# Performance work log

Hardware: AMD Instinct MI355X
Metric: run time of the kernel (lower is better)

Reference implementation:

```python
import jax, jax.numpy as jnp
import numpy as np

MUL0, MUL1 = 128, 64            # scalar (0e) and vector (1o) multiplicities
B = 8192                        # batch of nodes
SQRT3 = 3.0 ** 0.5
SQRT6 = 6.0 ** 0.5

# path normalization (e3nn 'component' irrep norm / 'element' path norm):
# coeff_ins = sqrt(dim(ir_out) / fan_in(i_out)), fan_in = sum_{ins -> i_out} mul1*mul2
A_0E = (1.0 / (MUL0 * MUL0 + MUL1 * MUL1)) ** 0.5   # paths (0,0,0)+(1,1,0)
A_1O = (3.0 / (MUL0 * MUL1 + MUL1 * MUL0)) ** 0.5   # paths (0,1,1)+(1,0,1)
A_1E = (3.0 / (MUL1 * MUL1)) ** 0.5                  # path  (1,1,1)


def _levi_civita():
    eps = np.zeros((3, 3, 3), dtype=np.float32)
    eps[0, 1, 2] = eps[1, 2, 0] = eps[2, 0, 1] = 1.0
    eps[0, 2, 1] = eps[2, 1, 0] = eps[1, 0, 2] = -1.0
    return jnp.asarray(eps)


def setup_inputs() -> dict:
    key = jax.random.key(0)
    ks = jax.random.split(key, 7)
    return {
        "x1": jax.random.normal(ks[0], (B, MUL0 + 3 * MUL1), dtype=jnp.float32),
        "x2": jax.random.normal(ks[1], (B, MUL0 + 3 * MUL1), dtype=jnp.float32),
        "w000": jax.random.normal(ks[2], (MUL0, MUL0, MUL0), dtype=jnp.float32),
        "w011": jax.random.normal(ks[3], (MUL0, MUL1, MUL1), dtype=jnp.float32),
        "w101": jax.random.normal(ks[4], (MUL1, MUL0, MUL1), dtype=jnp.float32),
        "w110": jax.random.normal(ks[5], (MUL1, MUL1, MUL0), dtype=jnp.float32),
        "w111": jax.random.normal(ks[6], (MUL1, MUL1, MUL1), dtype=jnp.float32),
    }


def reference(x1, x2, w000, w011, w101, w110, w111):
    b = x1.shape[0]
    # split irreps: scalars [b, 128], vectors [b, 64, 3]
    s1, v1 = x1[:, :MUL0], x1[:, MUL0:].reshape(b, MUL1, 3)
    s2, v2 = x2[:, :MUL0], x2[:, MUL0:].reshape(b, MUL1, 3)

    # 0e output: 0e x 0e -> 0e (w3j = 1) and 1o x 1o -> 0e (w3j = delta/sqrt3)
    out0 = A_0E * (
        jnp.einsum("uvw,bu,bv->bw", w000, s1, s2)
        + jnp.einsum("uvw,bui,bvi->bw", w110, v1, v2) / SQRT3
    )

    # 1o output: 0e x 1o -> 1o and 1o x 0e -> 1o (w3j = delta/sqrt3)
    out1o = (A_1O / SQRT3) * (
        jnp.einsum("uvw,bu,bvi->bwi", w011, s1, v2)
        + jnp.einsum("uvw,bui,bv->bwi", w101, v1, s2)
    )

    # 1e output: 1o x 1o -> 1e (w3j = levi-civita / sqrt6)
    eps = _levi_civita()
    out1e = (A_1E / SQRT6) * jnp.einsum("uvw,bui,bvj,ijk->bwk", w111, v1, v2, eps)

    return jnp.concatenate(
        [out0, out1o.reshape(b, -1), out1e.reshape(b, -1)], axis=-1
    )  # [b, 128 + 192 + 192] = [b, 512]
```

## Files before the change

### kernel.cpp

```cpp
#include <hip/hip_runtime.h>
#include <stdint.h>


typedef _Float16 f16;
typedef f16 f16x8 __attribute__((ext_vector_type(8)));
typedef float f32x4 __attribute__((ext_vector_type(4)));
typedef int i32x4 __attribute__((ext_vector_type(4)));

#define OFF_W000 0u
#define OFF_W110 2097152u
#define OFF_W011 2621440u
#define OFF_W101 3145728u
#define OFF_W111 3670016u
#define OFF_XS1  3932160u
#define OFF_XS2  4980736u
#define OFF_XV1  6029312u
#define OFF_XV2  7602176u
#define OFF_S0A  9175040u
#define OFF_S0B  10223616u
#define OFF_S1O  13369344u
#define WS_ELEMS 14942208u

#define SC_0E 0.006987712429686843f
#define SC_1O 0.0078125f
#define SC_1E 0.011048543456039806f

__global__ void tile_all_k(const float* __restrict__ w000, const float* __restrict__ w011,
                           const float* __restrict__ w101, const float* __restrict__ w110,
                           const float* __restrict__ w111, const float* __restrict__ x1,
                           const float* __restrict__ x2, f16* __restrict__ ws)
{
  unsigned tid = blockIdx.x*256u + threadIdx.x;
  if (tid < 2097152u) {
    unsigned e=tid&7u, n=(tid>>3)&63u, q=(tid>>9)&3u, p=(tid>>11)&1u,
             u=(tid>>12)&127u, vh=(tid>>19)&1u, h=(tid>>20)&1u;
    unsigned v = vh*64u + p*32u + q*8u + e;
    ws[OFF_W000+tid] = (f16)w000[u*16384u + v*128u + h*64u + n];
    return;
  }
  tid -= 2097152u;
  if (tid < 524288u) {
    unsigned e=tid&7u, n=(tid>>3)&63u, q=(tid>>9)&3u, p=(tid>>11)&1u,
             u=(tid>>12)&63u, h=(tid>>18)&1u;
    unsigned v = p*32u + q*8u + e;
    ws[OFF_W110+tid] = (f16)(w110[u*8192u + v*128u + h*64u + n] * 0.5773502691896258f);
    return;
  }
  tid -= 524288u;
  if (tid < 524288u) {
    unsigned e=tid&7u, n=(tid>>3)&63u, q=(tid>>9)&3u, p=(tid>>11)&1u, u=tid>>12;
    unsigned v = p*32u + q*8u + e;
    ws[OFF_W011+tid] = (f16)w011[u*4096u + v*64u + n];
    return;
  }
  tid -= 524288u;
  if (tid < 524288u) {
    unsigned e=tid&7u, n=(tid>>3)&63u, q=(tid>>9)&3u, p=(tid>>11)&1u, u=tid>>12;
    unsigned v = p*32u + q*8u + e;
    ws[OFF_W101+tid] = (f16)w101[v*8192u + u*64u + n];
    return;
  }
  tid -= 524288u;
  if (tid < 262144u) {
    unsigned e=tid&7u, n=(tid>>3)&63u, q=(tid>>9)&3u, p=(tid>>11)&1u, u=tid>>12;
    unsigned v = p*32u + q*8u + e;
    ws[OFF_W111+tid] = (f16)w111[u*4096u + v*64u + n];
    return;
  }
  tid -= 262144u;
  if (tid < 1048576u) {
    unsigned e=tid&7u, r=(tid>>3)&127u, uo=(tid>>10)&15u, rt=tid>>14;
    ws[OFF_XS1+tid] = (f16)x1[(rt*128u+r)*320u + uo*8u + e];
    return;
  }
  tid -= 1048576u;
  if (tid < 1572864u) {
    unsigned e=tid&7u, r=(tid>>3)&127u, ov=(tid>>10)&7u, rest=tid>>13;
    unsigned i=rest%3u, rt=rest/3u;
    ws[OFF_XV1+tid] = (f16)x1[(rt*128u+r)*320u + 128u + (ov*8u+e)*3u + i];
    return;
  }
  tid -= 1572864u;
  if (tid < 1048576u) {
    unsigned e=tid&7u, r=(tid>>3)&127u, uo=(tid>>10)&15u, rt=tid>>14;
    ws[OFF_XS2+tid] = (f16)x2[(rt*128u+r)*320u + uo*8u + e];
    return;
  }
  tid -= 1048576u;
  {
    unsigned e=tid&7u, r=(tid>>3)&127u, ov=(tid>>10)&7u, rest=tid>>13;
    unsigned i=rest%3u, rt=rest/3u;
    ws[OFF_XV2+tid] = (f16)x2[(rt*128u+r)*320u + 128u + (ov*8u+e)*3u + i];
  }
}

#define GLD16(g,l) __builtin_amdgcn_global_load_lds( \
    (const __attribute__((address_space(1))) unsigned int*)(g), \
    (__attribute__((address_space(3))) unsigned int*)(l), 16, 0, 0)

#define WAITV(n) asm volatile("s_waitcnt vmcnt(" #n ")" ::: "memory")

template<bool NEG, int SS>
__device__ __forceinline__ void run_phase(const f16* __restrict__ Wt,
    const f16* __restrict__ aW, const f16* __restrict__ bW, int bRow,
    f16* sWw, f16* sAw, f32x4 (&acc)[4][4], int lane)
{
  constexpr int M = SS*8;
  const int q = lane >> 4, r15 = lane & 15;

  f16x8 br[4][2];
#pragma unroll
  for (int mt=0; mt<4; ++mt)
#pragma unroll
    for (int o=0; o<2; ++o)
      br[mt][o] = *(const f16x8*)(bW + (o*4+q)*1024 + (bRow + mt*16 + r15)*8);
#pragma unroll
  for (int mt=0; mt<4; ++mt)
#pragma unroll
    for (int o=0; o<2; ++o) {
      i32x4 tmp = __builtin_bit_cast(i32x4, br[mt][o]);
      asm volatile("" :: "v"(tmp));
    }

  auto stPair = [&](int p, int slot){
    const char* s = (const char*)Wt + (size_t)p*8192;
    char* d = (char*)sWw + slot*8192;
#pragma unroll
    for (int c=0; c<8; ++c)
      GLD16(s + c*1024 + lane*16, d + c*1024);
  };
  auto stA = [&](int ss2){
    GLD16((const char*)(aW + ss2*1024) + lane*16, (char*)sAw + (ss2&1)*1024);
  };

  stPair(0,0); stA(0); stPair(1,1);

  f16x8 aR[4];
#pragma unroll 1
  for (int ss = 0; ss < SS; ++ss) {
#pragma unroll
    for (int kc = 0; kc < 8; ++kc) {
      const int t = ss*8 + kc;
      if (kc == 7) { if (ss+1 < SS) { WAITV(9); } else { WAITV(0); } }
      else         { WAITV(8); }
      if (kc == 0) {
#pragma unroll
        for (int mt=0; mt<4; ++mt)
          aR[mt] = *(const f16x8*)(sAw + (ss&1)*512 + (mt*16+r15)*8);
      }
      __builtin_amdgcn_s_setprio(1);
#pragma unroll
      for (int p=0; p<2; ++p) {
        f16x8 af[4];
#pragma unroll
        for (int mt=0; mt<4; ++mt) {
          f16 av = aR[mt][kc];
          if constexpr (NEG) av = -av;
          af[mt] = av * br[mt][p];
        }
#pragma unroll
        for (int nt=0; nt<4; ++nt) {
          f16x8 bw = *(const f16x8*)(sWw + (kc&1)*4096 + p*2048 + (q*64 + nt*16 + r15)*8);
#pragma unroll
          for (int mt=0; mt<4; ++mt)
            acc[mt][nt] = __builtin_amdgcn_mfma_f32_16x16x32_f16(af[mt], bw, acc[mt][nt], 0,0,0);
        }
      }
      __builtin_amdgcn_s_setprio(0);
      __builtin_amdgcn_sched_barrier(0);
      if (kc == 6 && ss+1 < SS) stA(ss+1);
      if (t + 2 < M) stPair(t+2, kc&1);
    }
  }
}

__global__ __launch_bounds__(256, 2)
void tp_main(f16* __restrict__ ws, float* __restrict__ out)
{
  __shared__ f16 smem[36864];
  const int lane = threadIdx.x & 63, wid = threadIdx.x >> 6;
  f16* sWw = smem + wid*8192;
  f16* sAw = smem + 32768 + wid*1024;
  const int q = lane >> 4, r15 = lane & 15;
  const int sub = wid >> 1, rh = wid & 1;

  f32x4 acc[4][4];
#pragma unroll
  for (int a=0;a<4;++a)
#pragma unroll
    for (int b=0;b<4;++b) acc[a][b] = (f32x4){0.f,0.f,0.f,0.f};

  const int bid = blockIdx.x;

#define STORE_DIRECT(base_col_expr, SC)                                   \
  _Pragma("unroll")                                                       \
  for (int mt=0;mt<4;++mt)                                                \
    _Pragma("unroll")                                                     \
    for (int nt=0;nt<4;++nt)                                              \
      _Pragma("unroll")                                                   \
      for (int rg=0;rg<4;++rg)                                            \
        out[(rowb+mt*16+q*4+rg)*512 + (base_col_expr)] = (SC)*acc[mt][nt][rg];

#define STORE_SLAB(slab, stride, col_expr, SC)                            \
  _Pragma("unroll")                                                       \
  for (int mt=0;mt<4;++mt)                                                \
    _Pragma("unroll")                                                     \
    for (int nt=0;nt<4;++nt)                                              \
      _Pragma("unroll")                                                   \
      for (int rg=0;rg<4;++rg)                                            \
        (slab)[(rowb+mt*16+q*4+rg)*(stride) + (col_expr)] = (f16)((SC)*acc[mt][nt][rg]);

  if (bid < 128) {
    const int rtp = bid >> 2, vh = (bid >> 1) & 1, h = bid & 1;
    const int rtt = rtp*2 + sub;
    const f16* aW = ws + OFF_XS1 + rtt*16384 + rh*512;
    const f16* bW = ws + OFF_XS2 + rtt*16384 + vh*8192;
    const f16* Wt = ws + OFF_W000 + h*1048576u + vh*524288u;
    run_phase<false,16>(Wt, aW, bW, rh*64, sWw, sAw, acc, lane);
    const int rowb = rtt*128 + rh*64;
    if (vh == 0) { STORE_DIRECT(h*64+nt*16+r15, SC_0E) }
    else { f16* slab = ws + OFF_S0A; STORE_SLAB(slab, 128, h*64+nt*16+r15, SC_0E) }
  } else if (bid < 224) {
    const int id = bid-128, i = id%3, rtp = id/3;
    const int rtt = rtp*2 + sub;
    const f16* aW = ws + OFF_XS1 + rtt*16384 + rh*512;
    const f16* bW = ws + OFF_XV2 + (rtt*3+i)*8192;
    run_phase<false,16>(ws + OFF_W011, aW, bW, rh*64, sWw, sAw, acc, lane);
    const int rowb = rtt*128 + rh*64;
    STORE_DIRECT(128 + 3*(nt*16+r15) + i, SC_1O)
  } else if (bid < 320) {
    const int id = bid-224, i = id%3, rtp = id/3;
    const int rtt = rtp*2 + sub;
    const f16* aW = ws + OFF_XS2 + rtt*16384 + rh*512;
    const f16* bW = ws + OFF_XV1 + (rtt*3+i)*8192;
    run_phase<false,16>(ws + OFF_W101, aW, bW, rh*64, sWw, sAw, acc, lane);
    const int rowb = rtt*128 + rh*64;
    f16* slab = ws + OFF_S1O;
    STORE_SLAB(slab, 192, 3*(nt*16+r15) + i, SC_1O)
  } else if (bid < 416) {
    const int id = bid-320, kk = id%3, rtp = id/3;
    int i = kk+1; if (i>2) i-=3;
    int j = kk+2; if (j>2) j-=3;
    const int rtt = rtp*2 + sub;
    run_phase<false,8>(ws + OFF_W111,
        ws + OFF_XV1 + (rtt*3+i)*8192 + rh*512, ws + OFF_XV2 + (rtt*3+j)*8192,
        rh*64, sWw, sAw, acc, lane);
    run_phase<true,8>(ws + OFF_W111,
        ws + OFF_XV1 + (rtt*3+j)*8192 + rh*512, ws + OFF_XV2 + (rtt*3+i)*8192,
        rh*64, sWw, sAw, acc, lane);
    const int rowb = rtt*128 + rh*64;
    STORE_DIRECT(320 + 3*(nt*16+r15) + kk, SC_1E)
  } else {
    const int id = bid-416, i = id%3, h = (id/3)&1, rtp = id/6;
    const int rtt = rtp*2 + sub;
    const f16* aW = ws + OFF_XV1 + (rtt*3+i)*8192 + rh*512;
    const f16* bW = ws + OFF_XV2 + (rtt*3+i)*8192;
    run_phase<false,8>(ws + OFF_W110 + h*262144u, aW, bW, rh*64, sWw, sAw, acc, lane);
    const int rowb = rtt*128 + rh*64;
    f16* slab = ws + OFF_S0B + (unsigned)i*1048576u;
    STORE_SLAB(slab, 128, h*64+nt*16+r15, SC_0E)
  }
#undef STORE_DIRECT
#undef STORE_SLAB
}

__global__ void ep_add(const f16* __restrict__ ws, float* __restrict__ out)
{
  unsigned tid = blockIdx.x*256u + threadIdx.x;
  if (tid < 1048576u) {
    unsigned r = tid>>7, c = tid&127u;
    float s = (float)ws[OFF_S0A+tid] + (float)ws[OFF_S0B+tid]
            + (float)ws[OFF_S0B+1048576u+tid] + (float)ws[OFF_S0B+2097152u+tid];
    out[r*512u+c] += s;
  } else {
    unsigned t2 = tid - 1048576u;
    unsigned r = t2/192u, c = t2 - r*192u;
    out[r*512u+128u+c] += (float)ws[OFF_S1O+t2];
  }
}

extern "C" void kernel_launch(void* const* d_in, const int* in_sizes, int n_in,
                              void* d_out, int out_size, void* d_ws, size_t ws_size,
                              hipStream_t stream)
{
  const float* x1   = (const float*)d_in[0];
  const float* x2   = (const float*)d_in[1];
  const float* w000 = (const float*)d_in[2];
  const float* w011 = (const float*)d_in[3];
  const float* w101 = (const float*)d_in[4];
  const float* w110 = (const float*)d_in[5];
  const float* w111 = (const float*)d_in[6];
  float* out = (float*)d_out;
  f16* ws   = (f16*)d_ws;

  if (ws_size < (size_t)WS_ELEMS * 2) return;

  tile_all_k<<<35840, 256, 0, stream>>>(w000, w011, w101, w110, w111, x1, x2, ws);
  tp_main<<<608, 256, 0, stream>>>(ws, out);
  ep_add<<<10240, 256, 0, stream>>>(ws, out);
}
```

Measured before the change: 157.6 us.

## Stream weights directly into registers with single-wave blocks, drop LDS staging

Replaces the LDS-staged weight pipeline (global_load_lds with double buffering across 4 waves) with per-wave direct global loads into a 4-deep register ring. The main kernel now launches many 64-thread blocks. Inputs are relaid out with rows contiguous across all nodes, and the w000 path is no longer split over the v halves, which removes the S0A partial slab. The epilogue reduction is rewritten for the new slab layout. The aim is to remove LDS traffic and barrier waits and to improve load balance, at the cost of more global and L2 traffic per wave and higher register pressure.

```diff
diff --git a/kernel.cpp b/kernel.cpp
--- a/kernel.cpp
+++ b/kernel.cpp
@@ -5,7 +5,6 @@
 typedef _Float16 f16;
 typedef f16 f16x8 __attribute__((ext_vector_type(8)));
 typedef float f32x4 __attribute__((ext_vector_type(4)));
-typedef int i32x4 __attribute__((ext_vector_type(4)));
 
 #define OFF_W000 0u
 #define OFF_W110 2097152u
@@ -16,10 +15,9 @@
 #define OFF_XS2  4980736u
 #define OFF_XV1  6029312u
 #define OFF_XV2  7602176u
-#define OFF_S0A  9175040u
-#define OFF_S0B  10223616u
-#define OFF_S1O  13369344u
-#define WS_ELEMS 14942208u
+#define OFF_S110 9175040u
+#define OFF_S101 12320768u
+#define WS_ELEMS 13893632u
 
 #define SC_0E 0.006987712429686843f
 #define SC_1O 0.0078125f
@@ -32,16 +30,16 @@
 {
   unsigned tid = blockIdx.x*256u + threadIdx.x;
   if (tid < 2097152u) {
-    unsigned e=tid&7u, n=(tid>>3)&63u, q=(tid>>9)&3u, p=(tid>>11)&1u,
-             u=(tid>>12)&127u, vh=(tid>>19)&1u, h=(tid>>20)&1u;
-    unsigned v = vh*64u + p*32u + q*8u + e;
+    unsigned e=tid&7u, n=(tid>>3)&63u, q=(tid>>9)&3u, vq=(tid>>11)&3u,
+             u=(tid>>13)&127u, h=tid>>20;
+    unsigned v = vq*32u + q*8u + e;
     ws[OFF_W000+tid] = (f16)w000[u*16384u + v*128u + h*64u + n];
     return;
   }
   tid -= 2097152u;
   if (tid < 524288u) {
     unsigned e=tid&7u, n=(tid>>3)&63u, q=(tid>>9)&3u, p=(tid>>11)&1u,
-             u=(tid>>12)&63u, h=(tid>>18)&1u;
+             u=(tid>>12)&63u, h=tid>>18;
     unsigned v = p*32u + q*8u + e;
     ws[OFF_W110+tid] = (f16)(w110[u*8192u + v*128u + h*64u + n] * 0.5773502691896258f);
     return;
@@ -69,196 +67,182 @@
   }
   tid -= 262144u;
   if (tid < 1048576u) {
-    unsigned e=tid&7u, r=(tid>>3)&127u, uo=(tid>>10)&15u, rt=tid>>14;
-    ws[OFF_XS1+tid] = (f16)x1[(rt*128u+r)*320u + uo*8u + e];
+    unsigned e=tid&7u, r=(tid>>3)&8191u, o=tid>>16;
+    ws[OFF_XS1+tid] = (f16)x1[r*320u + o*8u + e];
+    return;
+  }
+  tid -= 1048576u;
+  if (tid < 1048576u) {
+    unsigned e=tid&7u, r=(tid>>3)&8191u, o=tid>>16;
+    ws[OFF_XS2+tid] = (f16)x2[r*320u + o*8u + e];
     return;
   }
   tid -= 1048576u;
   if (tid < 1572864u) {
-    unsigned e=tid&7u, r=(tid>>3)&127u, ov=(tid>>10)&7u, rest=tid>>13;
-    unsigned i=rest%3u, rt=rest/3u;
-    ws[OFF_XV1+tid] = (f16)x1[(rt*128u+r)*320u + 128u + (ov*8u+e)*3u + i];
+    unsigned e=tid&7u, r=(tid>>3)&8191u, o=(tid>>16)&7u, i=tid>>19;
+    ws[OFF_XV1+tid] = (f16)x1[r*320u + 128u + (o*8u+e)*3u + i];
     return;
   }
   tid -= 1572864u;
-  if (tid < 1048576u) {
-    unsigned e=tid&7u, r=(tid>>3)&127u, uo=(tid>>10)&15u, rt=tid>>14;
-    ws[OFF_XS2+tid] = (f16)x2[(rt*128u+r)*320u + uo*8u + e];
-    return;
-  }
-  tid -= 1048576u;
   {
-    unsigned e=tid&7u, r=(tid>>3)&127u, ov=(tid>>10)&7u, rest=tid>>13;
-    unsigned i=rest%3u, rt=rest/3u;
-    ws[OFF_XV2+tid] = (f16)x2[(rt*128u+r)*320u + 128u + (ov*8u+e)*3u + i];
-  }
-}
-
-#define GLD16(g,l) __builtin_amdgcn_global_load_lds( \
-    (const __attribute__((address_space(1))) unsigned int*)(g), \
-    (__attribute__((address_space(3))) unsigned int*)(l), 16, 0, 0)
-
-#define WAITV(n) asm volatile("s_waitcnt vmcnt(" #n ")" ::: "memory")
-
-template<bool NEG, int SS>
-__device__ __forceinline__ void run_phase(const f16* __restrict__ Wt,
-    const f16* __restrict__ aW, const f16* __restrict__ bW, int bRow,
-    f16* sWw, f16* sAw, f32x4 (&acc)[4][4], int lane)
-{
-  constexpr int M = SS*8;
+    unsigned e=tid&7u, r=(tid>>3)&8191u, o=(tid>>16)&7u, i=tid>>19;
+    ws[OFF_XV2+tid] = (f16)x2[r*320u + 128u + (o*8u+e)*3u + i];
+  }
+}
+
+template<int VQ2, int SS, bool NEG>
+__device__ __forceinline__ void run_stream(
+    const f16* __restrict__ W, const f16* __restrict__ aP,
+    const f16* __restrict__ bP, int rowb, int lane, f32x4 (&acc)[4][4])
+{
+  constexpr int L = 8*VQ2;
   const int q = lane >> 4, r15 = lane & 15;
-
-  f16x8 br[4][2];
+  const int rbase = rowb + r15;
+
+  f16x8 br[4][VQ2];
 #pragma unroll
   for (int mt=0; mt<4; ++mt)
 #pragma unroll
-    for (int o=0; o<2; ++o)
-      br[mt][o] = *(const f16x8*)(bW + (o*4+q)*1024 + (bRow + mt*16 + r15)*8);
+    for (int vq=0; vq<VQ2; ++vq)
+      br[mt][vq] = *(const f16x8*)(bP + (unsigned)((vq*4+q)*8192 + rbase + mt*16)*8u);
+
+  const f16* Wl = W + (q*64 + r15)*8;
+  f16x8 ring[4][4];
+#pragma unroll
+  for (int s=0; s<4; ++s)
+#pragma unroll
+    for (int nt=0; nt<4; ++nt)
+      ring[s][nt] = *(const f16x8*)(Wl + s*2048 + nt*128);
+
+  f16x8 aR[4], aRn[4];
 #pragma unroll
   for (int mt=0; mt<4; ++mt)
-#pragma unroll
-    for (int o=0; o<2; ++o) {
-      i32x4 tmp = __builtin_bit_cast(i32x4, br[mt][o]);
-      asm volatile("" :: "v"(tmp));
+    aR[mt] = *(const f16x8*)(aP + (unsigned)(rbase + mt*16)*8u);
+
+#pragma unroll 1
+  for (int ss = 0; ss < SS-1; ++ss) {
+    const f16* Wss = Wl + (unsigned)(ss*L)*2048u;
+    const f16* An  = aP + (unsigned)((ss+1)*8192)*8u;
+#pragma unroll
+    for (int kc = 0; kc < L; ++kc) {
+      if (kc == L-6) {
+#pragma unroll
+        for (int mt=0; mt<4; ++mt)
+          aRn[mt] = *(const f16x8*)(An + (unsigned)(rbase + mt*16)*8u);
+      }
+      f16x8 af[4];
+#pragma unroll
+      for (int mt=0; mt<4; ++mt) {
+        f16 av = aR[mt][kc/VQ2];
+        if constexpr (NEG) av = -av;
+        af[mt] = av * br[mt][kc%VQ2];
+      }
+#pragma unroll
+      for (int nt=0; nt<4; ++nt)
+#pragma unroll
+        for (int mt=0; mt<4; ++mt)
+          acc[mt][nt] = __builtin_amdgcn_mfma_f32_16x16x32_f16(af[mt], ring[kc&3][nt], acc[mt][nt], 0,0,0);
+#pragma unroll
+      for (int nt=0; nt<4; ++nt)
+        ring[kc&3][nt] = *(const f16x8*)(Wss + (kc+4)*2048 + nt*128);
     }
-
-  auto stPair = [&](int p, int slot){
-    const char* s = (const char*)Wt + (size_t)p*8192;
-    char* d = (char*)sWw + slot*8192;
-#pragma unroll
-    for (int c=0; c<8; ++c)
-      GLD16(s + c*1024 + lane*16, d + c*1024);
-  };
-  auto stA = [&](int ss2){
-    GLD16((const char*)(aW + ss2*1024) + lane*16, (char*)sAw + (ss2&1)*1024);
-  };
-
-  stPair(0,0); stA(0); stPair(1,1);
-
-  f16x8 aR[4];
-#pragma unroll 1
-  for (int ss = 0; ss < SS; ++ss) {
-#pragma unroll
-    for (int kc = 0; kc < 8; ++kc) {
-      const int t = ss*8 + kc;
-      if (kc == 7) { if (ss+1 < SS) { WAITV(9); } else { WAITV(0); } }
-      else         { WAITV(8); }
-      if (kc == 0) {
+#pragma unroll
+    for (int mt=0; mt<4; ++mt) aR[mt] = aRn[mt];
+  }
+  {
+    const f16* Wss = Wl + (unsigned)((SS-1)*L)*2048u;
+#pragma unroll
+    for (int kc = 0; kc < L; ++kc) {
+      f16x8 af[4];
+#pragma unroll
+      for (int mt=0; mt<4; ++mt) {
+        f16 av = aR[mt][kc/VQ2];
+        if constexpr (NEG) av = -av;
+        af[mt] = av * br[mt][kc%VQ2];
+      }
+#pragma unroll
+      for (int nt=0; nt<4; ++nt)
 #pragma unroll
         for (int mt=0; mt<4; ++mt)
-          aR[mt] = *(const f16x8*)(sAw + (ss&1)*512 + (mt*16+r15)*8);
-      }
-      __builtin_amdgcn_s_setprio(1);
-#pragma unroll
-      for (int p=0; p<2; ++p) {
-        f16x8 af[4];
-#pragma unroll
-        for (int mt=0; mt<4; ++mt) {
-          f16 av = aR[mt][kc];
-          if constexpr (NEG) av = -av;
-          af[mt] = av * br[mt][p];
-        }
-#pragma unroll
-        for (int nt=0; nt<4; ++nt) {
-          f16x8 bw = *(const f16x8*)(sWw + (kc&1)*4096 + p*2048 + (q*64 + nt*16 + r15)*8);
-#pragma unroll
-          for (int mt=0; mt<4; ++mt)
-            acc[mt][nt] = __builtin_amdgcn_mfma_f32_16x16x32_f16(af[mt], bw, acc[mt][nt], 0,0,0);
-        }
-      }
-      __builtin_amdgcn_s_setprio(0);
-      __builtin_amdgcn_sched_barrier(0);
-      if (kc == 6 && ss+1 < SS) stA(ss+1);
-      if (t + 2 < M) stPair(t+2, kc&1);
+          acc[mt][nt] = __builtin_amdgcn_mfma_f32_16x16x32_f16(af[mt], ring[kc&3][nt], acc[mt][nt], 0,0,0);
+      if (kc < L-4) {
+#pragma unroll
+        for (int nt=0; nt<4; ++nt)
+          ring[kc&3][nt] = *(const f16x8*)(Wss + (kc+4)*2048 + nt*128);
+      }
     }
   }
 }
 
-__global__ __launch_bounds__(256, 2)
+__global__ __launch_bounds__(64, 2)
 void tp_main(f16* __restrict__ ws, float* __restrict__ out)
 {
-  __shared__ f16 smem[36864];
-  const int lane = threadIdx.x & 63, wid = threadIdx.x >> 6;
-  f16* sWw = smem + wid*8192;
-  f16* sAw = smem + 32768 + wid*1024;
+  const int lane = threadIdx.x & 63;
   const int q = lane >> 4, r15 = lane & 15;
-  const int sub = wid >> 1, rh = wid & 1;
 
   f32x4 acc[4][4];
 #pragma unroll
-  for (int a=0;a<4;++a)
-#pragma unroll
-    for (int b=0;b<4;++b) acc[a][b] = (f32x4){0.f,0.f,0.f,0.f};
-
-  const int bid = blockIdx.x;
-
-#define STORE_DIRECT(base_col_expr, SC)                                   \
+  for (int a=0; a<4; ++a)
+#pragma unroll
+    for (int b=0; b<4; ++b) acc[a][b] = (f32x4){0.f,0.f,0.f,0.f};
+
+  const int x = blockIdx.x & 7, r = blockIdx.x >> 3;
+
+#define STORE_DIRECT(col_expr, SC)                                        \
   _Pragma("unroll")                                                       \
   for (int mt=0;mt<4;++mt)                                                \
     _Pragma("unroll")                                                     \
     for (int nt=0;nt<4;++nt)                                              \
       _Pragma("unroll")                                                   \
       for (int rg=0;rg<4;++rg)                                            \
-        out[(rowb+mt*16+q*4+rg)*512 + (base_col_expr)] = (SC)*acc[mt][nt][rg];
-
-#define STORE_SLAB(slab, stride, col_expr, SC)                            \
+        out[(unsigned)(rowb+mt*16+q*4+rg)*512u + (unsigned)(col_expr)] = (SC)*acc[mt][nt][rg];
+
+#define STORE_SLAB(base, SC)                                              \
   _Pragma("unroll")                                                       \
   for (int mt=0;mt<4;++mt)                                                \
     _Pragma("unroll")                                                     \
     for (int nt=0;nt<4;++nt)                                              \
       _Pragma("unroll")                                                   \
       for (int rg=0;rg<4;++rg)                                            \
-        (slab)[(rowb+mt*16+q*4+rg)*(stride) + (col_expr)] = (f16)((SC)*acc[mt][nt][rg]);
-
-  if (bid < 128) {
-    const int rtp = bid >> 2, vh = (bid >> 1) & 1, h = bid & 1;
-    const int rtt = rtp*2 + sub;
-    const f16* aW = ws + OFF_XS1 + rtt*16384 + rh*512;
-    const f16* bW = ws + OFF_XS2 + rtt*16384 + vh*8192;
-    const f16* Wt = ws + OFF_W000 + h*1048576u + vh*524288u;
-    run_phase<false,16>(Wt, aW, bW, rh*64, sWw, sAw, acc, lane);
-    const int rowb = rtt*128 + rh*64;
-    if (vh == 0) { STORE_DIRECT(h*64+nt*16+r15, SC_0E) }
-    else { f16* slab = ws + OFF_S0A; STORE_SLAB(slab, 128, h*64+nt*16+r15, SC_0E) }
-  } else if (bid < 224) {
-    const int id = bid-128, i = id%3, rtp = id/3;
-    const int rtt = rtp*2 + sub;
-    const f16* aW = ws + OFF_XS1 + rtt*16384 + rh*512;
-    const f16* bW = ws + OFF_XV2 + (rtt*3+i)*8192;
-    run_phase<false,16>(ws + OFF_W011, aW, bW, rh*64, sWw, sAw, acc, lane);
-    const int rowb = rtt*128 + rh*64;
+        ws[(base) + (unsigned)(rowb+mt*16+q*4+rg)*64u + (unsigned)(nt*16+r15)] \
+            = (f16)((SC)*acc[mt][nt][rg]);
+
+  if (r < 32) {
+    const int j = x*32 + r, h = j >> 7, rg = j & 127;
+    const int rowb = rg*64;
+    run_stream<4,16,false>(ws + OFF_W000 + (unsigned)h*1048576u,
+                           ws + OFF_XS1, ws + OFF_XS2, rowb, lane, acc);
+    STORE_DIRECT(h*64 + nt*16 + r15, SC_0E)
+  } else if (r < 80) {
+    const int j = x*48 + (r-32), i = j/128, rg = j%128;
+    const int rowb = rg*64;
+    run_stream<2,16,false>(ws + OFF_W011, ws + OFF_XS1,
+                           ws + OFF_XV2 + (unsigned)i*524288u, rowb, lane, acc);
     STORE_DIRECT(128 + 3*(nt*16+r15) + i, SC_1O)
-  } else if (bid < 320) {
-    const int id = bid-224, i = id%3, rtp = id/3;
-    const int rtt = rtp*2 + sub;
-    const f16* aW = ws + OFF_XS2 + rtt*16384 + rh*512;
-    const f16* bW = ws + OFF_XV1 + (rtt*3+i)*8192;
-    run_phase<false,16>(ws + OFF_W101, aW, bW, rh*64, sWw, sAw, acc, lane);
-    const int rowb = rtt*128 + rh*64;
-    f16* slab = ws + OFF_S1O;
-    STORE_SLAB(slab, 192, 3*(nt*16+r15) + i, SC_1O)
-  } else if (bid < 416) {
-    const int id = bid-320, kk = id%3, rtp = id/3;
+  } else if (r < 128) {
+    const int j = x*48 + (r-80), i = j/128, rg = j%128;
+    const int rowb = rg*64;
+    run_stream<2,16,false>(ws + OFF_W101, ws + OFF_XS2,
+                           ws + OFF_XV1 + (unsigned)i*524288u, rowb, lane, acc);
+    STORE_SLAB(OFF_S101 + (unsigned)i*524288u, SC_1O)
+  } else if (r < 176) {
+    const int j = x*48 + (r-128), kk = j/128, rg = j%128;
+    const int rowb = rg*64;
     int i = kk+1; if (i>2) i-=3;
-    int j = kk+2; if (j>2) j-=3;
-    const int rtt = rtp*2 + sub;
-    run_phase<false,8>(ws + OFF_W111,
-        ws + OFF_XV1 + (rtt*3+i)*8192 + rh*512, ws + OFF_XV2 + (rtt*3+j)*8192,
-        rh*64, sWw, sAw, acc, lane);
-    run_phase<true,8>(ws + OFF_W111,
-        ws + OFF_XV1 + (rtt*3+j)*8192 + rh*512, ws + OFF_XV2 + (rtt*3+i)*8192,
-        rh*64, sWw, sAw, acc, lane);
-    const int rowb = rtt*128 + rh*64;
+    int jj = kk+2; if (jj>2) jj-=3;
+    run_stream<2,8,false>(ws + OFF_W111, ws + OFF_XV1 + (unsigned)i*524288u,
+                          ws + OFF_XV2 + (unsigned)jj*524288u, rowb, lane, acc);
+    run_stream<2,8,true>(ws + OFF_W111, ws + OFF_XV1 + (unsigned)jj*524288u,
+                         ws + OFF_XV2 + (unsigned)i*524288u, rowb, lane, acc);
     STORE_DIRECT(320 + 3*(nt*16+r15) + kk, SC_1E)
   } else {
-    const int id = bid-416, i = id%3, h = (id/3)&1, rtp = id/6;
-    const int rtt = rtp*2 + sub;
-    const f16* aW = ws + OFF_XV1 + (rtt*3+i)*8192 + rh*512;
-    const f16* bW = ws + OFF_XV2 + (rtt*3+i)*8192;
-    run_phase<false,8>(ws + OFF_W110 + h*262144u, aW, bW, rh*64, sWw, sAw, acc, lane);
-    const int rowb = rtt*128 + rh*64;
-    f16* slab = ws + OFF_S0B + (unsigned)i*1048576u;
-    STORE_SLAB(slab, 128, h*64+nt*16+r15, SC_0E)
+    const int j = x*96 + (r-176);
+    const int h = j/384, t2 = j%384, i = t2/128, rg = t2%128;
+    const int rowb = rg*64;
+    run_stream<2,8,false>(ws + OFF_W110 + (unsigned)h*262144u,
+                          ws + OFF_XV1 + (unsigned)i*524288u,
+                          ws + OFF_XV2 + (unsigned)i*524288u, rowb, lane, acc);
+    STORE_SLAB(OFF_S110 + (unsigned)(i*2+h)*524288u, SC_0E)
   }
 #undef STORE_DIRECT
 #undef STORE_SLAB
@@ -267,15 +251,17 @@
 __global__ void ep_add(const f16* __restrict__ ws, float* __restrict__ out)
 {
   unsigned tid = blockIdx.x*256u + threadIdx.x;
-  if (tid < 1048576u) {
-    unsigned r = tid>>7, c = tid&127u;
-    float s = (float)ws[OFF_S0A+tid] + (float)ws[OFF_S0B+tid]
-            + (float)ws[OFF_S0B+1048576u+tid] + (float)ws[OFF_S0B+2097152u+tid];
-    out[r*512u+c] += s;
+  unsigned r = tid/320u, c = tid - r*320u;
+  if (c < 128u) {
+    unsigned h = c>>6, cc = c&63u;
+    float s = (float)ws[OFF_S110 + (0u*2u+h)*524288u + r*64u + cc]
+            + (float)ws[OFF_S110 + (1u*2u+h)*524288u + r*64u + cc]
+            + (float)ws[OFF_S110 + (2u*2u+h)*524288u + r*64u + cc];
+    out[r*512u + c] += s;
   } else {
-    unsigned t2 = tid - 1048576u;
-    unsigned r = t2/192u, c = t2 - r*192u;
-    out[r*512u+128u+c] += (float)ws[OFF_S1O+t2];
+    unsigned t = c - 128u;
+    unsigned n = (t*21846u)>>16, i = t - n*3u;
+    out[r*512u + c] += (float)ws[OFF_S101 + i*524288u + r*64u + n];
   }
 }
 
@@ -296,6 +282,6 @@
   if (ws_size < (size_t)WS_ELEMS * 2) return;
 
   tile_all_k<<<35840, 256, 0, stream>>>(w000, w011, w101, w110, w111, x1, x2, ws);
-  tp_main<<<608, 256, 0, stream>>>(ws, out);
+  tp_main<<<2176, 64, 0, stream>>>(ws, out);
   ep_add<<<10240, 256, 0, stream>>>(ws, out);
 }
```

New measurement: 308.5 us. 1.96x slower.
